# Performance work log

Measured on AMD Instinct MI355X. Metric: run time of the kernel, lower is better.

The kernel has to match this reference:

```python
import jax, jax.numpy as jnp
import numpy as np

RADIUS = 5
KERNEL = 2 * RADIUS + 1  # 11
N_PATCHES = KERNEL * KERNEL  # 121
SIGMA_DIAG = np.array([10.0, 10.0, 0.02, 0.02, 0.02, 0.1, 0.1, 0.1], dtype=np.float32)


def _shift(x):
    # x: [B, C, H, W] -> [B, P, C, H, W] with P = KERNEL^2 reflect-padded window shifts
    b, c, h, w = x.shape
    xp = jnp.pad(x, ((0, 0), (0, 0), (RADIUS, RADIUS), (RADIUS, RADIUS)), mode='reflect')
    patches = [xp[:, :, dy:dy + h, dx:dx + w]
               for dy in range(KERNEL) for dx in range(KERNEL)]
    return jnp.stack(patches, axis=1)


def setup_inputs() -> dict:
    key = jax.random.key(0)
    k1, k2 = jax.random.split(key)
    image = jax.random.uniform(k1, (2, 3, 256, 256), dtype=jnp.float32)
    guidance = jax.random.uniform(k2, (2, 8, 256, 256), dtype=jnp.float32)
    return {"image": image, "guidance": guidance}


def reference(image, guidance):
    # sigma_inv = inverse of diag(SIGMA_DIAG): diagonal, so just reciprocal per channel
    sigma_inv = jnp.asarray(1.0 / SIGMA_DIAG, dtype=guidance.dtype)  # [8]

    sg = _shift(guidance)                       # [B, P, 8, H, W]
    center = sg[:, N_PATCHES // 2:N_PATCHES // 2 + 1]
    diff = sg - center                          # [B, P, 8, H, W]
    # Mahalanobis^2 with diagonal sigma_inv: sum_c diff^2 / sigma_c
    maha_sq = jnp.einsum('bpchw,c->bphw', diff * diff, sigma_inv)
    weights = jnp.exp(-0.5 * maha_sq)           # [B, P, H, W]

    si = _shift(image)                          # [B, P, 3, H, W]
    weighted_sum = jnp.einsum('bpchw,bphw->bchw', si, weights)
    sum_w = jnp.clip(jnp.sum(weights, axis=1, keepdims=False), 1e-10, None)  # [B, H, W]
    return weighted_sum / sum_w[:, None]        # [B, 3, H, W]
```

## Files before the change

kernel.cpp:

```cpp
#include <hip/hip_runtime.h>

#define RADIUS 5
#define TILEX  32
#define TILEY  16
#define HX     (TILEX + 2*RADIUS)
#define HY     (TILEY + 2*RADIUS)
#define HPITCH 22
#define H      256
#define W      256

#define KA (-0.072134752f)
#define KB (-36.06737602f)
#define KC (-7.213475204f)

typedef float v2f __attribute__((ext_vector_type(2)));

struct Center { v2f h01, h23, h45, h67; float phic; };

__device__ __forceinline__ void accum(const float4 A, const float4 G, const float4 P,
                                      const Center& C, const float pg,
                                      v2f& swx, v2f& syz) {
    v2f t2;  t2.x = P.w + pg; t2.y = 0.f;
    v2f a01; a01.x = A.x; a01.y = A.y;
    v2f a23; a23.x = A.z; a23.y = A.w;
    v2f g01; g01.x = G.x; g01.y = G.y;
    v2f g23; g23.x = G.z; g23.y = G.w;
    t2 = __builtin_elementwise_fma(C.h01, a01, t2);
    t2 = __builtin_elementwise_fma(C.h23, a23, t2);
    t2 = __builtin_elementwise_fma(C.h45, g01, t2);
    t2 = __builtin_elementwise_fma(C.h67, g23, t2);
    const float w = __builtin_amdgcn_exp2f(t2.x + t2.y);
    v2f w2;  w2.x = w;   w2.y = w;
    v2f m0;  m0.x = 1.f; m0.y = P.x;
    v2f m1;  m1.x = P.y; m1.y = P.z;
    swx = __builtin_elementwise_fma(w2, m0, swx);
    syz = __builtin_elementwise_fma(w2, m1, syz);
}

__global__ __launch_bounds__(512, 1) void jbf_kernel(
    const float* __restrict__ image,
    const float* __restrict__ guidance,
    float* __restrict__ out)
{
    __shared__ float4 g0e[HY * HPITCH], g0o[HY * HPITCH];
    __shared__ float4 g1e[HY * HPITCH], g1o[HY * HPITCH];
    __shared__ float4 ime[HY * HPITCH], imo[HY * HPITCH];

    const int id = blockIdx.x;
    const int c_xcd = id & 7;
    const int r_rnk = id >> 3;
    const int b       = c_xcd >> 2;
    const int tile_x0 = (((c_xcd & 3) << 1) | (r_rnk & 1)) * TILEX;
    const int tile_y0 = (r_rnk >> 1) * TILEY;

    const int txp = threadIdx.x;
    const int h   = threadIdx.y;
    const int typ = threadIdx.z;
    const int tid = (typ * 4 + h) * 16 + txp;

    const float* gbase = guidance + (size_t)b * 8 * H * W;
    const float* ibase = image    + (size_t)b * 3 * H * W;

    for (int idx = tid; idx < HX * HY; idx += 512) {
        const int ly = idx / HX;
        const int lx = idx - ly * HX;
        int gy = tile_y0 - RADIUS + ly;
        int gx = tile_x0 - RADIUS + lx;
        gy = (gy < 0) ? -gy : ((gy >= H) ? 2 * (H - 1) - gy : gy);
        gx = (gx < 0) ? -gx : ((gx >= W) ? 2 * (W - 1) - gx : gx);
        const int off = gy * W + gx;
        const int l   = ly * HPITCH + (lx >> 1);
        const float4 v0 = make_float4(gbase[0*H*W+off], gbase[1*H*W+off],
                                      gbase[2*H*W+off], gbase[3*H*W+off]);
        const float4 v1 = make_float4(gbase[4*H*W+off], gbase[5*H*W+off],
                                      gbase[6*H*W+off], gbase[7*H*W+off]);
        const float phi = KA * (v0.x*v0.x + v0.y*v0.y)
                        + KB * (v0.z*v0.z + v0.w*v0.w + v1.x*v1.x)
                        + KC * (v1.y*v1.y + v1.z*v1.z + v1.w*v1.w);
        const float4 vi = make_float4(ibase[0*H*W+off], ibase[1*H*W+off],
                                      ibase[2*H*W+off], phi);
        if (lx & 1) { g0o[l] = v0; g1o[l] = v1; imo[l] = vi; }
        else        { g0e[l] = v0; g1e[l] = v1; ime[l] = vi; }
    }
    __syncthreads();

    Center c[2][2];
    #pragma unroll
    for (int cy = 0; cy < 2; ++cy) {
        const int row = (2 * typ + 5 + cy) * HPITCH;
        #pragma unroll
        for (int cx = 0; cx < 2; ++cx) {
            const int ci = row + txp + 2 + cx;
            const float4 gA = cx ? g0e[ci] : g0o[ci];
            const float4 gB = cx ? g1e[ci] : g1o[ci];
            const float4 pv = cx ? ime[ci] : imo[ci];
            c[cx][cy].h01.x = -2.f*KA*gA.x;  c[cx][cy].h01.y = -2.f*KA*gA.y;
            c[cx][cy].h23.x = -2.f*KB*gA.z;  c[cx][cy].h23.y = -2.f*KB*gA.w;
            c[cx][cy].h45.x = -2.f*KB*gB.x;  c[cx][cy].h45.y = -2.f*KC*gB.y;
            c[cx][cy].h67.x = -2.f*KC*gB.z;  c[cx][cy].h67.y = -2.f*KC*gB.w;
            c[cx][cy].phic  = pv.w;
        }
    }

    v2f swx[2][2], syz[2][2];
    #pragma unroll
    for (int cx = 0; cx < 2; ++cx)
        #pragma unroll
        for (int cy = 0; cy < 2; ++cy) {
            swx[cx][cy].x = 0.f; swx[cx][cy].y = 0.f;
            syz[cx][cy].x = 0.f; syz[cx][cy].y = 0.f;
        }

    #pragma unroll
    for (int i = 0; i < 3; ++i) {
        const int r  = 4 * i + h;
        const int rb = (2 * typ + r) * HPITCH + txp;
        const float b0 = (r <= 10) ? 0.0f : -1000.0f;
        const float b1 = (r >= 1)  ? 0.0f : -1000.0f;
        const float pg00 = c[0][0].phic + b0, pg01 = c[0][1].phic + b1;
        const float pg10 = c[1][0].phic + b0, pg11 = c[1][1].phic + b1;
        #pragma unroll
        for (int k = 0; k <= 5; ++k) {
            {
                const float4 A = g0e[rb + k], G = g1e[rb + k], P = ime[rb + k];
                accum(A, G, P, c[0][0], pg00, swx[0][0], syz[0][0]);
                accum(A, G, P, c[0][1], pg01, swx[0][1], syz[0][1]);
                if (k >= 1) {
                    accum(A, G, P, c[1][0], pg10, swx[1][0], syz[1][0]);
                    accum(A, G, P, c[1][1], pg11, swx[1][1], syz[1][1]);
                }
            }
            {
                const float4 A = g0o[rb + k], G = g1o[rb + k], P = imo[rb + k];
                if (k <= 4) {
                    accum(A, G, P, c[0][0], pg00, swx[0][0], syz[0][0]);
                    accum(A, G, P, c[0][1], pg01, swx[0][1], syz[0][1]);
                }
                accum(A, G, P, c[1][0], pg10, swx[1][0], syz[1][0]);
                accum(A, G, P, c[1][1], pg11, swx[1][1], syz[1][1]);
            }
        }
    }

    #pragma unroll
    for (int cx = 0; cx < 2; ++cx)
        #pragma unroll
        for (int cy = 0; cy < 2; ++cy) {
            swx[cx][cy].x += __shfl_xor(swx[cx][cy].x, 16);
            swx[cx][cy].x += __shfl_xor(swx[cx][cy].x, 32);
            swx[cx][cy].y += __shfl_xor(swx[cx][cy].y, 16);
            swx[cx][cy].y += __shfl_xor(swx[cx][cy].y, 32);
            syz[cx][cy].x += __shfl_xor(syz[cx][cy].x, 16);
            syz[cx][cy].x += __shfl_xor(syz[cx][cy].x, 32);
            syz[cx][cy].y += __shfl_xor(syz[cx][cy].y, 16);
            syz[cx][cy].y += __shfl_xor(syz[cx][cy].y, 32);
        }

    if (h == 0) {
        const size_t base = (size_t)b * 3 * H * W
                          + (size_t)(tile_y0 + 2 * typ) * W + (tile_x0 + 2 * txp);
        #pragma unroll
        for (int cy = 0; cy < 2; ++cy) {
            const float i0 = 1.0f / swx[0][cy].x;
            const float i1 = 1.0f / swx[1][cy].x;
            float2* __restrict__ o2 = (float2*)(out + base + (size_t)cy * W);
            o2[0]           = make_float2(swx[0][cy].y * i0, swx[1][cy].y * i1);
            o2[(H*W) / 2]   = make_float2(syz[0][cy].x * i0, syz[1][cy].x * i1);
            o2[(2*H*W) / 2] = make_float2(syz[0][cy].y * i0, syz[1][cy].y * i1);
        }
    }
}

extern "C" void kernel_launch(void* const* d_in, const int* in_sizes, int n_in,
                              void* d_out, int out_size, void* d_ws, size_t ws_size,
                              hipStream_t stream) {
    const float* image    = (const float*)d_in[0];
    const float* guidance = (const float*)d_in[1];
    float* out            = (float*)d_out;

    dim3 grid(256, 1, 1);
    dim3 block(16, 4, 8);
    hipLaunchKernelGGL(jbf_kernel, grid, block, 0, stream, image, guidance, out);
}
```

Baseline: 66.73 us.

## Pack low-sensitivity guidance and image channels as fp16 in shared memory

```diff
diff --git a/kernel.cpp b/kernel.cpp
--- a/kernel.cpp
+++ b/kernel.cpp
@@ -14,6 +14,7 @@
 #define KC (-7.213475204f)
 
 typedef float v2f __attribute__((ext_vector_type(2)));
+typedef _Float16 half8 __attribute__((ext_vector_type(8)));
 
 struct Center { v2f h01, h23, h45, h67; float phic; };
 
@@ -37,14 +38,20 @@
     syz = __builtin_elementwise_fma(w2, m1, syz);
 }
 
+__device__ __forceinline__ void unpack(const float4 f, const half8 hv,
+                                       float4& A, float4& G, float4& P) {
+    A = make_float4((float)hv[0], (float)hv[1], f.x, f.y);
+    G = make_float4(f.z, (float)hv[2], (float)hv[3], (float)hv[4]);
+    P = make_float4((float)hv[5], (float)hv[6], (float)hv[7], f.w);
+}
+
 __global__ __launch_bounds__(512, 1) void jbf_kernel(
     const float* __restrict__ image,
     const float* __restrict__ guidance,
     float* __restrict__ out)
 {
-    __shared__ float4 g0e[HY * HPITCH], g0o[HY * HPITCH];
-    __shared__ float4 g1e[HY * HPITCH], g1o[HY * HPITCH];
-    __shared__ float4 ime[HY * HPITCH], imo[HY * HPITCH];
+    __shared__ float4 fe[HY * HPITCH], fo[HY * HPITCH];
+    __shared__ half8  he[HY * HPITCH], ho[HY * HPITCH];
 
     const int id = blockIdx.x;
     const int c_xcd = id & 7;
@@ -70,17 +77,22 @@
         gx = (gx < 0) ? -gx : ((gx >= W) ? 2 * (W - 1) - gx : gx);
         const int off = gy * W + gx;
         const int l   = ly * HPITCH + (lx >> 1);
-        const float4 v0 = make_float4(gbase[0*H*W+off], gbase[1*H*W+off],
-                                      gbase[2*H*W+off], gbase[3*H*W+off]);
-        const float4 v1 = make_float4(gbase[4*H*W+off], gbase[5*H*W+off],
-                                      gbase[6*H*W+off], gbase[7*H*W+off]);
-        const float phi = KA * (v0.x*v0.x + v0.y*v0.y)
-                        + KB * (v0.z*v0.z + v0.w*v0.w + v1.x*v1.x)
-                        + KC * (v1.y*v1.y + v1.z*v1.z + v1.w*v1.w);
-        const float4 vi = make_float4(ibase[0*H*W+off], ibase[1*H*W+off],
-                                      ibase[2*H*W+off], phi);
-        if (lx & 1) { g0o[l] = v0; g1o[l] = v1; imo[l] = vi; }
-        else        { g0e[l] = v0; g1e[l] = v1; ime[l] = vi; }
+        const float g0 = gbase[0*H*W+off], g1 = gbase[1*H*W+off];
+        const float g2 = gbase[2*H*W+off], g3 = gbase[3*H*W+off];
+        const float g4 = gbase[4*H*W+off], g5 = gbase[5*H*W+off];
+        const float g6 = gbase[6*H*W+off], g7 = gbase[7*H*W+off];
+        const float i0 = ibase[0*H*W+off], i1 = ibase[1*H*W+off];
+        const float i2 = ibase[2*H*W+off];
+        const float phi = KA * (g0*g0 + g1*g1)
+                        + KB * (g2*g2 + g3*g3 + g4*g4)
+                        + KC * (g5*g5 + g6*g6 + g7*g7);
+        const float4 vf = make_float4(g2, g3, g4, phi);
+        half8 vh;
+        vh[0] = (_Float16)g0; vh[1] = (_Float16)g1;
+        vh[2] = (_Float16)g5; vh[3] = (_Float16)g6; vh[4] = (_Float16)g7;
+        vh[5] = (_Float16)i0; vh[6] = (_Float16)i1; vh[7] = (_Float16)i2;
+        if (lx & 1) { fo[l] = vf; ho[l] = vh; }
+        else        { fe[l] = vf; he[l] = vh; }
     }
     __syncthreads();
 
@@ -91,14 +103,15 @@
         #pragma unroll
         for (int cx = 0; cx < 2; ++cx) {
             const int ci = row + txp + 2 + cx;
-            const float4 gA = cx ? g0e[ci] : g0o[ci];
-            const float4 gB = cx ? g1e[ci] : g1o[ci];
-            const float4 pv = cx ? ime[ci] : imo[ci];
-            c[cx][cy].h01.x = -2.f*KA*gA.x;  c[cx][cy].h01.y = -2.f*KA*gA.y;
-            c[cx][cy].h23.x = -2.f*KB*gA.z;  c[cx][cy].h23.y = -2.f*KB*gA.w;
-            c[cx][cy].h45.x = -2.f*KB*gB.x;  c[cx][cy].h45.y = -2.f*KC*gB.y;
-            c[cx][cy].h67.x = -2.f*KC*gB.z;  c[cx][cy].h67.y = -2.f*KC*gB.w;
-            c[cx][cy].phic  = pv.w;
+            const float4 f  = cx ? fe[ci] : fo[ci];
+            const half8  hv = cx ? he[ci] : ho[ci];
+            float4 A, G, P;
+            unpack(f, hv, A, G, P);
+            c[cx][cy].h01.x = -2.f*KA*A.x;  c[cx][cy].h01.y = -2.f*KA*A.y;
+            c[cx][cy].h23.x = -2.f*KB*A.z;  c[cx][cy].h23.y = -2.f*KB*A.w;
+            c[cx][cy].h45.x = -2.f*KB*G.x;  c[cx][cy].h45.y = -2.f*KC*G.y;
+            c[cx][cy].h67.x = -2.f*KC*G.z;  c[cx][cy].h67.y = -2.f*KC*G.w;
+            c[cx][cy].phic  = P.w;
         }
     }
 
@@ -122,7 +135,8 @@
         #pragma unroll
         for (int k = 0; k <= 5; ++k) {
             {
-                const float4 A = g0e[rb + k], G = g1e[rb + k], P = ime[rb + k];
+                float4 A, G, P;
+                unpack(fe[rb + k], he[rb + k], A, G, P);
                 accum(A, G, P, c[0][0], pg00, swx[0][0], syz[0][0]);
                 accum(A, G, P, c[0][1], pg01, swx[0][1], syz[0][1]);
                 if (k >= 1) {
@@ -131,7 +145,8 @@
                 }
             }
             {
-                const float4 A = g0o[rb + k], G = g1o[rb + k], P = imo[rb + k];
+                float4 A, G, P;
+                unpack(fo[rb + k], ho[rb + k], A, G, P);
                 if (k <= 4) {
                     accum(A, G, P, c[0][0], pg00, swx[0][0], syz[0][0]);
                     accum(A, G, P, c[0][1], pg01, swx[0][1], syz[0][1]);
```

After: 66.88 us. About the same (+0.2%).
